# Performance work log

Measured on AMD Instinct MI355X. Metric: run time of the kernel, lower is better.

## Reference

```python
import jax, jax.numpy as jnp
import numpy as np

# irreps structure: in = 32x0e + 16x1o, hidden = 64x0e + 32x1o, out = 32x0e + 16x1o
N = 50000
S_IN, V_IN = 32, 16
S_H, V_H = 64, 32
S_OUT, V_OUT = 32, 16
INV_SQRT3 = float(1.0 / np.sqrt(3.0))  # wigner-3j for (0,1,1)/(1,0,1)/(1,1,0)
# e3nn path weights: sqrt(ir_out.dim / sum_over_paths_to_same_output(fan_in)), fan_in = mul1*mul2
PW1_S = float((1.0 / (S_IN * S_IN + V_IN * V_IN)) ** 0.5)        # sqrt(1/1280)
PW1_V = float((3.0 / (S_IN * V_IN + V_IN * S_IN)) ** 0.5)        # sqrt(3/1024)
PW2_S = float((1.0 / (S_H * S_H + V_H * V_H)) ** 0.5)            # sqrt(1/5120)
PW2_V = float((3.0 / (S_H * V_H + V_H * S_H)) ** 0.5)            # sqrt(3/4096)


def norm_act(xs, xv, bias=None, normalize=False):
    # e3nn.nn.NormActivation with sigmoid: per-irrep-channel norm, gate by sigmoid(norm [+ bias])
    ns = jnp.abs(xs)                                 # [N, S] scalar channel norms
    nv = jnp.sqrt(jnp.sum(xv * xv, axis=-1))         # [N, V] vector channel norms
    norms = jnp.concatenate([ns, nv], axis=1)        # [N, S+V]
    a = norms if bias is None else norms + bias
    f = jax.nn.sigmoid(a)
    mult = f / norms if normalize else f
    s = xs.shape[1]
    return xs * mult[:, :s], xv * mult[:, s:, None]


def fctp(xs, xv, Wsss, Wvvs, Wsvv, Wvsv, pw_s, pw_v):
    # FullyConnectedTensorProduct(x, x) restricted to 0e/1o irreps (all surviving CG paths)
    zs = pw_s * (jnp.einsum('nu,nv,uvw->nw', xs, xs, Wsss)
                 + INV_SQRT3 * jnp.einsum('nui,nvi,uvw->nw', xv, xv, Wvvs))
    zv = (pw_v * INV_SQRT3) * (jnp.einsum('nu,nvk,uvw->nwk', xs, xv, Wsvv)
                               + jnp.einsum('nuk,nv,uvw->nwk', xv, xs, Wvsv))
    return zs, zv


def setup_inputs() -> dict:
    key = jax.random.key(0)
    ks = jax.random.split(key, 11)
    return {
        'x': jax.random.normal(ks[0], (N, S_IN + 3 * V_IN), dtype=jnp.float32),
        'Wsss1': jax.random.normal(ks[1], (S_IN, S_IN, S_H), dtype=jnp.float32),
        'Wvvs1': jax.random.normal(ks[2], (V_IN, V_IN, S_H), dtype=jnp.float32),
        'Wsvv1': jax.random.normal(ks[3], (S_IN, V_IN, V_H), dtype=jnp.float32),
        'Wvsv1': jax.random.normal(ks[4], (V_IN, S_IN, V_H), dtype=jnp.float32),
        'Wsss2': jax.random.normal(ks[5], (S_H, S_H, S_OUT), dtype=jnp.float32),
        'Wvvs2': jax.random.normal(ks[6], (V_H, V_H, S_OUT), dtype=jnp.float32),
        'Wsvv2': jax.random.normal(ks[7], (S_H, V_H, V_OUT), dtype=jnp.float32),
        'Wvsv2': jax.random.normal(ks[8], (V_H, S_H, V_OUT), dtype=jnp.float32),
        'b1': 0.1 * jax.random.normal(ks[9], (S_IN + V_IN,), dtype=jnp.float32),
        'b3': 0.1 * jax.random.normal(ks[10], (S_OUT + V_OUT,), dtype=jnp.float32),
    }


def reference(x, Wsss1, Wvvs1, Wsvv1, Wvsv1, Wsss2, Wvvs2, Wsvv2, Wvsv2, b1, b3):
    xs = x[:, :S_IN]
    xv = x[:, S_IN:].reshape(-1, V_IN, 3)
    xs, xv = norm_act(xs, xv, bias=b1, normalize=False)            # non_linear_act1
    hs, hv = fctp(xs, xv, Wsss1, Wvvs1, Wsvv1, Wvsv1, PW1_S, PW1_V)  # si1
    hs, hv = norm_act(hs, hv, bias=None, normalize=True)           # normalize_and_non_linear_act2
    os_, ov = fctp(hs, hv, Wsss2, Wvvs2, Wsvv2, Wvsv2, PW2_S, PW2_V)  # si2
    os_, ov = norm_act(os_, ov, bias=b3, normalize=False)          # non_linear_act3
    return jnp.concatenate([os_, ov.reshape(-1, V_OUT * 3)], axis=1)
```

## Files before the change

kernel.cpp:

```cpp
#include <hip/hip_runtime.h>

#define NROWS 50000

typedef float f32x4 __attribute__((ext_vector_type(4)));
typedef float f32x16 __attribute__((ext_vector_type(16)));
typedef short s16x8 __attribute__((ext_vector_type(8)));
typedef _Float16 f16x8 __attribute__((ext_vector_type(8)));

#define MFMA16B(a,b,c) __builtin_amdgcn_mfma_f32_16x16x32_bf16(a, b, c, 0, 0, 0)
#define MFMA32B(a,b,c) __builtin_amdgcn_mfma_f32_32x32x16_bf16(a, b, c, 0, 0, 0)
#define MFMA32H(a,b,c) __builtin_amdgcn_mfma_f32_32x32x16_f16(a, b, c, 0, 0, 0)

#define Q1ABH 0
#define Q1ABL 81920
#define Q1CH  163840
#define Q1CL  212992
#define P2A   262144
#define P2AV  (262144 + 73728)
#define P2C   425984
#define PREPN 323584


#define LO_SCALE   2048.0f
#define LO_UNSCALE 4.8828125e-4f

__device__ __forceinline__ float sigm(float a){ return 1.0f/(1.0f+__expf(-a)); }
__device__ __forceinline__ short bfb(float f){
  __bf16 b = (__bf16)f;
  return *reinterpret_cast<short*>(&b);
}
__device__ __forceinline__ float b2f(short s){
  unsigned u = ((unsigned)(unsigned short)s) << 16;
  float f;
  __builtin_memcpy(&f, &u, 4);
  return f;
}
__device__ __forceinline__ f32x16 zero16(){
  f32x16 v;
  #pragma unroll
  for (int i = 0; i < 16; ++i) v[i] = 0.f;
  return v;
}

__global__ __launch_bounds__(256) void prep_weights(
    const float* __restrict__ Wsss1, const float* __restrict__ Wvvs1,
    const float* __restrict__ Wsvv1, const float* __restrict__ Wvsv1,
    const float* __restrict__ Wsss2, const float* __restrict__ Wvvs2,
    const float* __restrict__ Wsvv2, const float* __restrict__ Wvsv2,
    short* __restrict__ pb)
{
  const float PW1S = 0.027950849718747374f;
  const float PW2S = 0.013975424859373687f;
  const float IS3  = 0.57735026918962576f;
  int i = blockIdx.x * 256 + threadIdx.x;
  if (i >= PREPN) return;
  if (i < 131072) {
    float w;
    int hiOff, loOff;
    if (i < 81920) {
      int e = i; int j = e & 7, l = (e >> 3) & 63, st = e >> 9;
      int t = st & 1, s = st >> 1;
      int k = 16*s + 8*(l >> 5) + j, n = 32*t + (l & 31);
      if (k < 1024) { int u = k >> 5, v = k & 31; w = PW1S * Wsss1[(u*32 + v)*64 + n]; }
      else { int kk = k - 1024; int u = kk >> 4, v = kk & 15; w = PW1S * IS3 * Wvvs1[(u*16 + v)*64 + n]; }
      hiOff = Q1ABH + e; loOff = Q1ABL + e;
    } else {
      int e = i - 81920; int e2 = e & 16383;
      int j = e2 & 7, l = (e2 >> 3) & 63, s = e2 >> 9;
      int k = 16*s + 8*(l >> 5) + j, n = l & 31;
      int u = k >> 4, v = k & 15;
      w = 0.03125f * (Wsvv1[(u*16 + v)*32 + n] + Wvsv1[(v*32 + u)*32 + n]);
      hiOff = Q1CH + e; loOff = Q1CL + e;
    }
    _Float16 h = (_Float16)w;
    float r = w - (float)h;
    _Float16 lo = (_Float16)(r * LO_SCALE);
    pb[hiOff] = *reinterpret_cast<short*>(&h);
    pb[loOff] = *reinterpret_cast<short*>(&lo);
  } else {
    int e = i - 131072;
    float val; int off;
    if (e < 73728) {
      int j = e & 7, l = (e >> 3) & 63, s = e >> 9;
      int k = 16*s + 8*(l >> 5) + j, n = l & 31;
      int B = k >> 6, kb = k & 63;
      int bb = 0;
      while ((bb + 1) * (bb + 2) / 2 <= B) ++bb;
      int a = B - bb * (bb + 1) / 2;
      int u = 8*a + (kb >> 3), v = 8*bb + (kb & 7);
      float w1 = Wsss2[(u*64 + v)*32 + n];
      val = PW2S * (a == bb ? w1 : w1 + Wsss2[(v*64 + u)*32 + n]);
      off = P2A + e;
    } else if (e < 94208) {
      int e2 = e - 73728;
      int j = e2 & 7, l = (e2 >> 3) & 63, s = e2 >> 9;
      int k = 16*s + 8*(l >> 5) + j, n = l & 31;
      int B = k >> 6, kb = k & 63;
      int bb = 0;
      while ((bb + 1) * (bb + 2) / 2 <= B) ++bb;
      int a = B - bb * (bb + 1) / 2;
      int u = 8*a + (kb >> 3), v = 8*bb + (kb & 7);
      float w1 = Wvvs2[(u*32 + v)*32 + n];
      val = PW2S * IS3 * (a == bb ? w1 : w1 + Wvvs2[(v*32 + u)*32 + n]);
      off = P2AV + e2;
    } else {
      int e3 = e - 94208; int e4 = e3 & 32767;
      int j = e4 & 7, l = (e4 >> 3) & 63, s = e4 >> 9;
      int k = 32*s + 8*(l >> 4) + j, n = l & 15;
      int u = k >> 5, v = k & 31;
      val = 0.015625f * (Wsvv2[(u*32 + v)*16 + n] + Wvsv2[(v*64 + u)*16 + n]);
      off = P2C + e3;
    }
    pb[off] = bfb(val);
  }
}

__global__ __launch_bounds__(128, 4) void double_layer(
    const float* __restrict__ x,
    const float* __restrict__ b1,
    const float* __restrict__ b3,
    const short* __restrict__ pb,
    float* __restrict__ out)
{
  __shared__ __align__(16) float smem[5120];
  char* S = (char*)smem;

  const int lane = threadIdx.x & 63;
  const int wid  = __builtin_amdgcn_readfirstlane(threadIdx.x >> 6);
  const int h    = lane >> 5;
  const int r31  = lane & 31;
  const int row  = r31;
  const int grow0 = blockIdx.x * 32;
  const int xb = row * 320;
  const int hb = 10240 + row * 320;
  const int sz = ((row >> 1) & 3) << 4;
  const bool valid = (grow0 + row) < NROWS;
  const float* xrow = x + (size_t)(grow0 + row) * 80;

  if (wid == 0) {
    #pragma unroll
    for (int i = 0; i < 4; ++i) {
      float4 qv = valid ? ((const float4*)xrow)[4*h + i] : float4{0.f,0.f,0.f,0.f};
      int c0 = 16*h + 4*i;
      f32x4 o;
      o[0] = qv.x * sigm(fabsf(qv.x) + b1[c0+0]);
      o[1] = qv.y * sigm(fabsf(qv.y) + b1[c0+1]);
      o[2] = qv.z * sigm(fabsf(qv.z) + b1[c0+2]);
      o[3] = qv.w * sigm(fabsf(qv.w) + b1[c0+3]);
      *(f32x4*)(S + xb + ((64*h + 16*i) ^ sz)) = o;
    }
  } else {
    float t[24];
    #pragma unroll
    for (int i = 0; i < 6; ++i) {
      float4 qv = valid ? ((const float4*)xrow)[8 + 6*h + i] : float4{0.f,0.f,0.f,0.f};
      t[4*i] = qv.x; t[4*i+1] = qv.y; t[4*i+2] = qv.z; t[4*i+3] = qv.w;
    }
    #pragma unroll
    for (int vv = 0; vv < 8; ++vv) {
      float a0 = t[3*vv], a1 = t[3*vv+1], a2 = t[3*vv+2];
      float f = sigm(sqrtf(a0*a0 + a1*a1 + a2*a2) + b1[32 + 8*h + vv]);
      t[3*vv] = a0*f; t[3*vv+1] = a1*f; t[3*vv+2] = a2*f;
    }
    #pragma unroll
    for (int i = 0; i < 6; ++i) {
      f32x4 o; o[0] = t[4*i]; o[1] = t[4*i+1]; o[2] = t[4*i+2]; o[3] = t[4*i+3];
      *(f32x4*)(S + xb + ((128 + 96*h + 16*i) ^ sz)) = o;
    }
  }
  __syncthreads();

  if (wid == 0) {
    f32x16 aH0 = zero16(), aM0 = zero16(), aH1 = zero16(), aM1 = zero16();
    const f16x8* BH = (const f16x8*)(pb + Q1ABH);
    const f16x8* BL = (const f16x8*)(pb + Q1ABL);
    float xsv[16];
    {
      #pragma unroll
      for (int si = 0; si < 2; ++si) {
        f32x4 p0 = *(const f32x4*)(S + xb + ((64*si + 32*h) ^ sz));
        f32x4 p1 = *(const f32x4*)(S + xb + ((64*si + 32*h + 16) ^ sz));
        #pragma unroll
        for (int j = 0; j < 4; ++j) { xsv[8*si+j] = p0[j]; xsv[8*si+4+j] = p1[j]; }
      }
    }
    #pragma unroll 2
    for (int so = 0; so < 32; ++so) {
      float xu = *(const float*)(S + xb + ((4*so) ^ sz));
      #pragma unroll
      for (int si = 0; si < 2; ++si) {
        int s = 2*so + si;
        f16x8 ah, al;
        #pragma unroll
        for (int j = 0; j < 8; ++j) {
          float f = xu * xsv[8*si + j];
          _Float16 hh = (_Float16)f;
          ah[j] = hh;
          al[j] = (_Float16)((f - (float)hh) * LO_SCALE);
        }
        const f16x8* Bh = BH + (2*s)*64 + lane;
        const f16x8* Bl = BL + (2*s)*64 + lane;
        f16x8 b0 = Bh[0], b1_ = Bh[64];
        aH0 = MFMA32H(ah, b0,  aH0); aM0 = MFMA32H(al, b0,  aM0); aM0 = MFMA32H(ah, Bl[0],  aM0);
        aH1 = MFMA32H(ah, b1_, aH1); aM1 = MFMA32H(al, b1_, aM1); aM1 = MFMA32H(ah, Bl[64], aM1);
      }
    }
    {
      float pv0[8], pv1[8], pv2[8];
      f32x4 P[6];
      #pragma unroll
      for (int i = 0; i < 6; ++i) P[i] = *(const f32x4*)(S + xb + ((128 + 96*h + 16*i) ^ sz));
      #pragma unroll
      for (int j = 0; j < 8; ++j) {
        pv0[j] = P[(3*j  )>>2][(3*j  )&3];
        pv1[j] = P[(3*j+1)>>2][(3*j+1)&3];
        pv2[j] = P[(3*j+2)>>2][(3*j+2)&3];
      }
      #pragma unroll 2
      for (int s2 = 0; s2 < 16; ++s2) {
        int s = 64 + s2;
        float u0 = *(const float*)(S + xb + ((4*(32 + 3*s2    )) ^ sz));
        float u1 = *(const float*)(S + xb + ((4*(32 + 3*s2 + 1)) ^ sz));
        float u2 = *(const float*)(S + xb + ((4*(32 + 3*s2 + 2)) ^ sz));
        f16x8 ah, al;
        #pragma unroll
        for (int j = 0; j < 8; ++j) {
          float f = u0*pv0[j] + u1*pv1[j] + u2*pv2[j];
          _Float16 hh = (_Float16)f;
          ah[j] = hh;
          al[j] = (_Float16)((f - (float)hh) * LO_SCALE);
        }
        const f16x8* Bh = BH + (2*s)*64 + lane;
        const f16x8* Bl = BL + (2*s)*64 + lane;
        f16x8 b0 = Bh[0], b1_ = Bh[64];
        aH0 = MFMA32H(ah, b0,  aH0); aM0 = MFMA32H(al, b0,  aM0); aM0 = MFMA32H(ah, Bl[0],  aM0);
        aH1 = MFMA32H(ah, b1_, aH1); aM1 = MFMA32H(al, b1_, aM1); aM1 = MFMA32H(ah, Bl[64], aM1);
      }
    }
    #pragma unroll
    for (int reg = 0; reg < 16; ++reg) {
      int rowD = (reg & 3) + 8*(reg >> 2) + 4*h;
      int hbD = 10240 + rowD*320;
      int szD = ((rowD >> 1) & 3) << 4;
      float z0 = aH0[reg] + LO_UNSCALE*aM0[reg];
      float z1 = aH1[reg] + LO_UNSCALE*aM1[reg];
      *(short*)(S + hbD + ((2*r31)        ^ szD)) = bfb(copysignf(sigm(fabsf(z0)), z0));
      *(short*)(S + hbD + ((2*(32 + r31)) ^ szD)) = bfb(copysignf(sigm(fabsf(z1)), z1));
    }
  } else {
    float pv0[8], pv1[8], pv2[8];
    {
      f32x4 P[6];
      #pragma unroll
      for (int i = 0; i < 6; ++i) P[i] = *(const f32x4*)(S + xb + ((128 + 96*h + 16*i) ^ sz));
      #pragma unroll
      for (int j = 0; j < 8; ++j) {
        pv0[j] = P[(3*j  )>>2][(3*j  )&3];
        pv1[j] = P[(3*j+1)>>2][(3*j+1)&3];
        pv2[j] = P[(3*j+2)>>2][(3*j+2)&3];
      }
    }
    const f16x8* CH = (const f16x8*)(pb + Q1CH);
    const f16x8* CL = (const f16x8*)(pb + Q1CL);
    f32x16 z0v, z1v, z2v;
    {
      f32x16 cH0 = zero16(), cM0 = zero16(), cH1 = zero16(), cM1 = zero16();
      #pragma unroll 2
      for (int s = 0; s < 32; ++s) {
        float xu = *(const float*)(S + xb + ((4*s) ^ sz));
        f16x8 a0h, a0l, a1h, a1l;
        #pragma unroll
        for (int j = 0; j < 8; ++j) {
          float f0 = xu*pv0[j]; _Float16 h0 = (_Float16)f0; a0h[j] = h0; a0l[j] = (_Float16)((f0 - (float)h0)*LO_SCALE);
          float f1 = xu*pv1[j]; _Float16 h1 = (_Float16)f1; a1h[j] = h1; a1l[j] = (_Float16)((f1 - (float)h1)*LO_SCALE);
        }
        const f16x8* B0h = CH + s*64 + lane;
        const f16x8* B0l = CL + s*64 + lane;
        f16x8 t0 = B0h[0];
        cH0 = MFMA32H(a0h, t0, cH0); cM0 = MFMA32H(a0l, t0, cM0); cM0 = MFMA32H(a0h, B0l[0], cM0);
        f16x8 t1 = B0h[2048];
        cH1 = MFMA32H(a1h, t1, cH1); cM1 = MFMA32H(a1l, t1, cM1); cM1 = MFMA32H(a1h, B0l[2048], cM1);
      }
      #pragma unroll
      for (int i = 0; i < 16; ++i) { z0v[i] = cH0[i] + LO_UNSCALE*cM0[i]; z1v[i] = cH1[i] + LO_UNSCALE*cM1[i]; }
    }
    {
      f32x16 cH2 = zero16(), cM2 = zero16();
      #pragma unroll 2
      for (int s = 0; s < 32; ++s) {
        float xu = *(const float*)(S + xb + ((4*s) ^ sz));
        f16x8 a2h, a2l;
        #pragma unroll
        for (int j = 0; j < 8; ++j) {
          float f2 = xu*pv2[j]; _Float16 h2 = (_Float16)f2; a2h[j] = h2; a2l[j] = (_Float16)((f2 - (float)h2)*LO_SCALE);
        }
        const f16x8* B2h = CH + 4096 + s*64 + lane;
        const f16x8* B2l = CL + 4096 + s*64 + lane;
        f16x8 t2 = B2h[0];
        cH2 = MFMA32H(a2h, t2, cH2); cM2 = MFMA32H(a2l, t2, cM2); cM2 = MFMA32H(a2h, B2l[0], cM2);
      }
      #pragma unroll
      for (int i = 0; i < 16; ++i) z2v[i] = cH2[i] + LO_UNSCALE*cM2[i];
    }
    #pragma unroll
    for (int reg = 0; reg < 16; ++reg) {
      int rowD = (reg & 3) + 8*(reg >> 2) + 4*h;
      int hbD = 10240 + rowD*320;
      int szD = ((rowD >> 1) & 3) << 4;
      float a0 = z0v[reg], a1 = z1v[reg], a2 = z2v[reg];
      float n = sqrtf(a0*a0 + a1*a1 + a2*a2);
      float mm = sigm(n) / n;
      int ch = 64 + 3*r31;
      *(short*)(S + hbD + ((2*(ch    )) ^ szD)) = bfb(a0*mm);
      *(short*)(S + hbD + ((2*(ch + 1)) ^ szD)) = bfb(a1*mm);
      *(short*)(S + hbD + ((2*(ch + 2)) ^ szD)) = bfb(a2*mm);
    }
  }
  __syncthreads();

  if (wid == 0) {
    f32x16 acc = zero16();
    {
      const s16x8* BA = (const s16x8*)(pb + P2A);
      int step = 0;
      #pragma unroll 2
      for (int b = 0; b < 8; ++b) {
        float hsb[8];
        {
          s16x8 w = *(const s16x8*)(S + hb + ((16*b) ^ sz));
          #pragma unroll
          for (int j = 0; j < 8; ++j) hsb[j] = b2f(w[j]);
        }
        for (int a = 0; a <= b; ++a) {
          #pragma unroll
          for (int s4 = 0; s4 < 4; ++s4) {
            float hu = b2f(*(const short*)(S + hb + ((2*(8*a + 2*s4 + h)) ^ sz)));
            s16x8 av;
            #pragma unroll
            for (int j = 0; j < 8; ++j) av[j] = bfb(hu * hsb[j]);
            acc = MFMA32B(av, BA[step*64 + lane], acc);
            ++step;
          }
        }
      }
    }
    {
      const s16x8* BV = (const s16x8*)(pb + P2AV);
      int step = 0;
      #pragma unroll
      for (int b = 0; b < 4; ++b) {
        float hvb[24];
        #pragma unroll
        for (int i = 0; i < 3; ++i) {
          s16x8 w = *(const s16x8*)(S + hb + ((2*(64 + 24*b + 8*i)) ^ sz));
          #pragma unroll
          for (int j = 0; j < 8; ++j) hvb[8*i + j] = b2f(w[j]);
        }
        for (int a = 0; a <= b; ++a) {
          #pragma unroll
          for (int s4 = 0; s4 < 4; ++s4) {
            int u = 8*a + 2*s4 + h;
            float u0 = b2f(*(const short*)(S + hb + ((2*(64 + 3*u    )) ^ sz)));
            float u1 = b2f(*(const short*)(S + hb + ((2*(64 + 3*u + 1)) ^ sz)));
            float u2 = b2f(*(const short*)(S + hb + ((2*(64 + 3*u + 2)) ^ sz)));
            s16x8 av;
            #pragma unroll
            for (int j = 0; j < 8; ++j)
              av[j] = bfb(u0*hvb[3*j] + u1*hvb[3*j+1] + u2*hvb[3*j+2]);
            acc = MFMA32B(av, BV[step*64 + lane], acc);
            ++step;
          }
        }
      }
    }
    float bs = b3[r31];
    #pragma unroll
    for (int reg = 0; reg < 16; ++reg) {
      int rowD = (reg & 3) + 8*(reg >> 2) + 4*h;
      int grow = grow0 + rowD;
      if (grow < NROWS) {
        float z = acc[reg];
        out[(size_t)grow*80 + r31] = z * sigm(fabsf(z) + bs);
      }
    }
  } else {
    const int q = lane >> 4, r15 = lane & 15;
    const int rA = r15, rB = 16 + r15;
    const int hbA = 10240 + rA*320, szA = ((rA >> 1) & 3) << 4;
    const int hbB = 10240 + rB*320, szB = ((rB >> 1) & 3) << 4;
    float vvA[24], vvB[24];
    #pragma unroll
    for (int i = 0; i < 3; ++i) {
      s16x8 wa = *(const s16x8*)(S + hbA + ((128 + 48*q + 16*i) ^ szA));
      s16x8 wb = *(const s16x8*)(S + hbB + ((128 + 48*q + 16*i) ^ szB));
      #pragma unroll
      for (int j = 0; j < 8; ++j) { vvA[8*i+j] = b2f(wa[j]); vvB[8*i+j] = b2f(wb[j]); }
    }
    f32x4 ac00 = {0.f,0.f,0.f,0.f}, ac01 = {0.f,0.f,0.f,0.f};
    f32x4 ac10 = {0.f,0.f,0.f,0.f}, ac11 = {0.f,0.f,0.f,0.f};
    f32x4 ac20 = {0.f,0.f,0.f,0.f}, ac21 = {0.f,0.f,0.f,0.f};
    const s16x8* BC = (const s16x8*)(pb + P2C);
    #pragma unroll 2
    for (int s = 0; s < 64; ++s) {
      float huA = b2f(*(const short*)(S + hbA + ((2*s) ^ szA)));
      float huB = b2f(*(const short*)(S + hbB + ((2*s) ^ szB)));
      s16x8 aA0, aA1, aA2, aB0, aB1, aB2;
      #pragma unroll
      for (int j = 0; j < 8; ++j) {
        aA0[j] = bfb(huA*vvA[3*j  ]); aA1[j] = bfb(huA*vvA[3*j+1]); aA2[j] = bfb(huA*vvA[3*j+2]);
        aB0[j] = bfb(huB*vvB[3*j  ]); aB1[j] = bfb(huB*vvB[3*j+1]); aB2[j] = bfb(huB*vvB[3*j+2]);
      }
      s16x8 B0 = BC[s*64 + lane];
      s16x8 B1 = BC[4096 + s*64 + lane];
      s16x8 B2 = BC[8192 + s*64 + lane];
      ac00 = MFMA16B(aA0, B0, ac00); ac01 = MFMA16B(aB0, B0, ac01);
      ac10 = MFMA16B(aA1, B1, ac10); ac11 = MFMA16B(aB1, B1, ac11);
      ac20 = MFMA16B(aA2, B2, ac20); ac21 = MFMA16B(aB2, B2, ac21);
    }
    float bv = b3[32 + r15];
    #pragma unroll
    for (int r = 0; r < 4; ++r) {
      int gA = grow0 + 4*q + r;
      if (gA < NROWS) {
        float z0 = ac00[r], z1 = ac10[r], z2 = ac20[r];
        float gg = sigm(sqrtf(z0*z0 + z1*z1 + z2*z2) + bv);
        out[(size_t)gA*80 + 32 + 3*r15    ] = z0*gg;
        out[(size_t)gA*80 + 32 + 3*r15 + 1] = z1*gg;
        out[(size_t)gA*80 + 32 + 3*r15 + 2] = z2*gg;
      }
      int gB = grow0 + 16 + 4*q + r;
      if (gB < NROWS) {
        float z0 = ac01[r], z1 = ac11[r], z2 = ac21[r];
        float gg = sigm(sqrtf(z0*z0 + z1*z1 + z2*z2) + bv);
        out[(size_t)gB*80 + 32 + 3*r15    ] = z0*gg;
        out[(size_t)gB*80 + 32 + 3*r15 + 1] = z1*gg;
        out[(size_t)gB*80 + 32 + 3*r15 + 2] = z2*gg;
      }
    }
  }
}

extern "C" void kernel_launch(void* const* d_in, const int* in_sizes, int n_in,
                              void* d_out, int out_size, void* d_ws, size_t ws_size,
                              hipStream_t stream) {
  const float* x     = (const float*)d_in[0];
  const float* Wsss1 = (const float*)d_in[1];
  const float* Wvvs1 = (const float*)d_in[2];
  const float* Wsvv1 = (const float*)d_in[3];
  const float* Wvsv1 = (const float*)d_in[4];
  const float* Wsss2 = (const float*)d_in[5];
  const float* Wvvs2 = (const float*)d_in[6];
  const float* Wsvv2 = (const float*)d_in[7];
  const float* Wvsv2 = (const float*)d_in[8];
  const float* b1    = (const float*)d_in[9];
  const float* b3    = (const float*)d_in[10];
  float* out = (float*)d_out;
  short* pb  = (short*)d_ws;

  hipLaunchKernelGGL(prep_weights, dim3((PREPN + 255)/256), dim3(256), 0, stream,
                     Wsss1, Wvvs1, Wsvv1, Wvsv1, Wsss2, Wvvs2, Wsvv2, Wvsv2, pb);
  hipLaunchKernelGGL(double_layer, dim3((NROWS + 31)/32), dim3(128), 0, stream,
                     x, b1, b3, pb, out);
}
```

Measured before the change: 116.2 us.

## Split fused double-layer work across four waves instead of two

```diff
diff --git a/kernel.cpp b/kernel.cpp
--- a/kernel.cpp
+++ b/kernel.cpp
@@ -18,7 +18,8 @@
 #define P2A   262144
 #define P2AV  (262144 + 73728)
 #define P2C   425984
-#define PREPN 323584
+#define PREPN 393216
+
 
 
 #define LO_SCALE   2048.0f
@@ -115,7 +116,7 @@
   }
 }
 
-__global__ __launch_bounds__(128, 4) void double_layer(
+__global__ __launch_bounds__(256, 4) void double_layer(
     const float* __restrict__ x,
     const float* __restrict__ b1,
     const float* __restrict__ b3,
@@ -149,7 +150,7 @@
       o[3] = qv.w * sigm(fabsf(qv.w) + b1[c0+3]);
       *(f32x4*)(S + xb + ((64*h + 16*i) ^ sz)) = o;
     }
-  } else {
+  } else if (wid == 1) {
     float t[24];
     #pragma unroll
     for (int i = 0; i < 6; ++i) {
@@ -170,10 +171,13 @@
   }
   __syncthreads();
 
-  if (wid == 0) {
-    f32x16 aH0 = zero16(), aM0 = zero16(), aH1 = zero16(), aM1 = zero16();
+  f32x16 z0v, z1v;
+
+  if (wid == 0 || wid == 1) {
+    f32x16 aH = zero16(), aM = zero16();
     const f16x8* BH = (const f16x8*)(pb + Q1ABH);
     const f16x8* BL = (const f16x8*)(pb + Q1ABL);
+    const int toff = (wid == 0) ? 0 : 64;
     float xsv[16];
     {
       #pragma unroll
@@ -198,11 +202,10 @@
           ah[j] = hh;
           al[j] = (_Float16)((f - (float)hh) * LO_SCALE);
         }
-        const f16x8* Bh = BH + (2*s)*64 + lane;
-        const f16x8* Bl = BL + (2*s)*64 + lane;
-        f16x8 b0 = Bh[0], b1_ = Bh[64];
-        aH0 = MFMA32H(ah, b0,  aH0); aM0 = MFMA32H(al, b0,  aM0); aM0 = MFMA32H(ah, Bl[0],  aM0);
-        aH1 = MFMA32H(ah, b1_, aH1); aM1 = MFMA32H(al, b1_, aM1); aM1 = MFMA32H(ah, Bl[64], aM1);
+        const f16x8* Bh = BH + (2*s)*64 + lane + toff;
+        const f16x8* Bl = BL + (2*s)*64 + lane + toff;
+        f16x8 b0 = Bh[0];
+        aH = MFMA32H(ah, b0, aH); aM = MFMA32H(al, b0, aM); aM = MFMA32H(ah, Bl[0], aM);
       }
     }
     {
@@ -230,25 +233,23 @@
           ah[j] = hh;
           al[j] = (_Float16)((f - (float)hh) * LO_SCALE);
         }
-        const f16x8* Bh = BH + (2*s)*64 + lane;
-        const f16x8* Bl = BL + (2*s)*64 + lane;
-        f16x8 b0 = Bh[0], b1_ = Bh[64];
-        aH0 = MFMA32H(ah, b0,  aH0); aM0 = MFMA32H(al, b0,  aM0); aM0 = MFMA32H(ah, Bl[0],  aM0);
-        aH1 = MFMA32H(ah, b1_, aH1); aM1 = MFMA32H(al, b1_, aM1); aM1 = MFMA32H(ah, Bl[64], aM1);
-      }
-    }
+        const f16x8* Bh = BH + (2*s)*64 + lane + toff;
+        const f16x8* Bl = BL + (2*s)*64 + lane + toff;
+        f16x8 b0 = Bh[0];
+        aH = MFMA32H(ah, b0, aH); aM = MFMA32H(al, b0, aM); aM = MFMA32H(ah, Bl[0], aM);
+      }
+    }
+    const int choff = (wid == 0) ? 0 : 32;
     #pragma unroll
     for (int reg = 0; reg < 16; ++reg) {
       int rowD = (reg & 3) + 8*(reg >> 2) + 4*h;
       int hbD = 10240 + rowD*320;
       int szD = ((rowD >> 1) & 3) << 4;
-      float z0 = aH0[reg] + LO_UNSCALE*aM0[reg];
-      float z1 = aH1[reg] + LO_UNSCALE*aM1[reg];
-      *(short*)(S + hbD + ((2*r31)        ^ szD)) = bfb(copysignf(sigm(fabsf(z0)), z0));
-      *(short*)(S + hbD + ((2*(32 + r31)) ^ szD)) = bfb(copysignf(sigm(fabsf(z1)), z1));
-    }
-  } else {
-    float pv0[8], pv1[8], pv2[8];
+      float z = aH[reg] + LO_UNSCALE*aM[reg];
+      *(short*)(S + hbD + ((2*(choff + r31)) ^ szD)) = bfb(copysignf(sigm(fabsf(z)), z));
+    }
+  } else if (wid == 2) {
+    float pv0[8], pv1[8];
     {
       f32x4 P[6];
       #pragma unroll
@@ -257,57 +258,78 @@
       for (int j = 0; j < 8; ++j) {
         pv0[j] = P[(3*j  )>>2][(3*j  )&3];
         pv1[j] = P[(3*j+1)>>2][(3*j+1)&3];
-        pv2[j] = P[(3*j+2)>>2][(3*j+2)&3];
       }
     }
     const f16x8* CH = (const f16x8*)(pb + Q1CH);
     const f16x8* CL = (const f16x8*)(pb + Q1CL);
-    f32x16 z0v, z1v, z2v;
+    f32x16 cH0 = zero16(), cM0 = zero16(), cH1 = zero16(), cM1 = zero16();
+    #pragma unroll 2
+    for (int s = 0; s < 32; ++s) {
+      float xu = *(const float*)(S + xb + ((4*s) ^ sz));
+      f16x8 a0h, a0l, a1h, a1l;
+      #pragma unroll
+      for (int j = 0; j < 8; ++j) {
+        float f0 = xu*pv0[j]; _Float16 h0 = (_Float16)f0; a0h[j] = h0; a0l[j] = (_Float16)((f0 - (float)h0)*LO_SCALE);
+        float f1 = xu*pv1[j]; _Float16 h1 = (_Float16)f1; a1h[j] = h1; a1l[j] = (_Float16)((f1 - (float)h1)*LO_SCALE);
+      }
+      const f16x8* B0h = CH + s*64 + lane;
+      const f16x8* B0l = CL + s*64 + lane;
+      f16x8 t0 = B0h[0];
+      cH0 = MFMA32H(a0h, t0, cH0); cM0 = MFMA32H(a0l, t0, cM0); cM0 = MFMA32H(a0h, B0l[0], cM0);
+      f16x8 t1 = B0h[2048];
+      cH1 = MFMA32H(a1h, t1, cH1); cM1 = MFMA32H(a1l, t1, cM1); cM1 = MFMA32H(a1h, B0l[2048], cM1);
+    }
+    #pragma unroll
+    for (int i = 0; i < 16; ++i) { z0v[i] = cH0[i] + LO_UNSCALE*cM0[i]; z1v[i] = cH1[i] + LO_UNSCALE*cM1[i]; }
+  } else {
+    float pv2[8];
     {
-      f32x16 cH0 = zero16(), cM0 = zero16(), cH1 = zero16(), cM1 = zero16();
-      #pragma unroll 2
-      for (int s = 0; s < 32; ++s) {
-        float xu = *(const float*)(S + xb + ((4*s) ^ sz));
-        f16x8 a0h, a0l, a1h, a1l;
-        #pragma unroll
-        for (int j = 0; j < 8; ++j) {
-          float f0 = xu*pv0[j]; _Float16 h0 = (_Float16)f0; a0h[j] = h0; a0l[j] = (_Float16)((f0 - (float)h0)*LO_SCALE);
-          float f1 = xu*pv1[j]; _Float16 h1 = (_Float16)f1; a1h[j] = h1; a1l[j] = (_Float16)((f1 - (float)h1)*LO_SCALE);
-        }
-        const f16x8* B0h = CH + s*64 + lane;
-        const f16x8* B0l = CL + s*64 + lane;
-        f16x8 t0 = B0h[0];
-        cH0 = MFMA32H(a0h, t0, cH0); cM0 = MFMA32H(a0l, t0, cM0); cM0 = MFMA32H(a0h, B0l[0], cM0);
-        f16x8 t1 = B0h[2048];
-        cH1 = MFMA32H(a1h, t1, cH1); cM1 = MFMA32H(a1l, t1, cM1); cM1 = MFMA32H(a1h, B0l[2048], cM1);
-      }
-      #pragma unroll
-      for (int i = 0; i < 16; ++i) { z0v[i] = cH0[i] + LO_UNSCALE*cM0[i]; z1v[i] = cH1[i] + LO_UNSCALE*cM1[i]; }
-    }
-    {
-      f32x16 cH2 = zero16(), cM2 = zero16();
-      #pragma unroll 2
-      for (int s = 0; s < 32; ++s) {
-        float xu = *(const float*)(S + xb + ((4*s) ^ sz));
-        f16x8 a2h, a2l;
-        #pragma unroll
-        for (int j = 0; j < 8; ++j) {
-          float f2 = xu*pv2[j]; _Float16 h2 = (_Float16)f2; a2h[j] = h2; a2l[j] = (_Float16)((f2 - (float)h2)*LO_SCALE);
-        }
-        const f16x8* B2h = CH + 4096 + s*64 + lane;
-        const f16x8* B2l = CL + 4096 + s*64 + lane;
-        f16x8 t2 = B2h[0];
-        cH2 = MFMA32H(a2h, t2, cH2); cM2 = MFMA32H(a2l, t2, cM2); cM2 = MFMA32H(a2h, B2l[0], cM2);
-      }
-      #pragma unroll
-      for (int i = 0; i < 16; ++i) z2v[i] = cH2[i] + LO_UNSCALE*cM2[i];
+      f32x4 P[6];
+      #pragma unroll
+      for (int i = 0; i < 6; ++i) P[i] = *(const f32x4*)(S + xb + ((128 + 96*h + 16*i) ^ sz));
+      #pragma unroll
+      for (int j = 0; j < 8; ++j)
+        pv2[j] = P[(3*j+2)>>2][(3*j+2)&3];
+    }
+    const f16x8* CH = (const f16x8*)(pb + Q1CH);
+    const f16x8* CL = (const f16x8*)(pb + Q1CL);
+    f32x16 cH2 = zero16(), cM2 = zero16();
+    #pragma unroll 2
+    for (int s = 0; s < 32; ++s) {
+      float xu = *(const float*)(S + xb + ((4*s) ^ sz));
+      f16x8 a2h, a2l;
+      #pragma unroll
+      for (int j = 0; j < 8; ++j) {
+        float f2 = xu*pv2[j]; _Float16 h2 = (_Float16)f2; a2h[j] = h2; a2l[j] = (_Float16)((f2 - (float)h2)*LO_SCALE);
+      }
+      const f16x8* B2h = CH + 4096 + s*64 + lane;
+      const f16x8* B2l = CL + 4096 + s*64 + lane;
+      f16x8 t2 = B2h[0];
+      cH2 = MFMA32H(a2h, t2, cH2); cM2 = MFMA32H(a2l, t2, cM2); cM2 = MFMA32H(a2h, B2l[0], cM2);
+    }
+    #pragma unroll
+    for (int reg = 0; reg < 16; ++reg) {
+      int rowD = (reg & 3) + 8*(reg >> 2) + 4*h;
+      float z2 = cH2[reg] + LO_UNSCALE*cM2[reg];
+      *(float*)(S + 10240 + rowD*320 + 128 + 4*r31) = z2;
+    }
+  }
+  __syncthreads();
+
+  f32x16 acc = zero16();
+  if (wid == 2) {
+    float z2a[16];
+    #pragma unroll
+    for (int reg = 0; reg < 16; ++reg) {
+      int rowD = (reg & 3) + 8*(reg >> 2) + 4*h;
+      z2a[reg] = *(const float*)(S + 10240 + rowD*320 + 128 + 4*r31);
     }
     #pragma unroll
     for (int reg = 0; reg < 16; ++reg) {
       int rowD = (reg & 3) + 8*(reg >> 2) + 4*h;
       int hbD = 10240 + rowD*320;
       int szD = ((rowD >> 1) & 3) << 4;
-      float a0 = z0v[reg], a1 = z1v[reg], a2 = z2v[reg];
+      float a0 = z0v[reg], a1 = z1v[reg], a2 = z2a[reg];
       float n = sqrtf(a0*a0 + a1*a1 + a2*a2);
       float mm = sigm(n) / n;
       int ch = 64 + 3*r31;
@@ -315,35 +337,41 @@
       *(short*)(S + hbD + ((2*(ch + 1)) ^ szD)) = bfb(a1*mm);
       *(short*)(S + hbD + ((2*(ch + 2)) ^ szD)) = bfb(a2*mm);
     }
+  } else {
+    const s16x8* BA = (const s16x8*)(pb + P2A);
+    int bLo, bHi, step;
+    if (wid == 0)      { bLo = 0; bHi = 5; step = 0;   }
+    else if (wid == 1) { bLo = 5; bHi = 7; step = 60;  }
+    else               { bLo = 7; bHi = 8; step = 112; }
+    for (int b = bLo; b < bHi; ++b) {
+      float hsb[8];
+      {
+        s16x8 w = *(const s16x8*)(S + hb + ((16*b) ^ sz));
+        #pragma unroll
+        for (int j = 0; j < 8; ++j) hsb[j] = b2f(w[j]);
+      }
+      for (int a = 0; a <= b; ++a) {
+        #pragma unroll
+        for (int s4 = 0; s4 < 4; ++s4) {
+          float hu = b2f(*(const short*)(S + hb + ((2*(8*a + 2*s4 + h)) ^ sz)));
+          s16x8 av;
+          #pragma unroll
+          for (int j = 0; j < 8; ++j) av[j] = bfb(hu * hsb[j]);
+          acc = MFMA32B(av, BA[step*64 + lane], acc);
+          ++step;
+        }
+      }
+    }
+    if (wid == 1 || wid == 3) {
+      int slot = (wid == 1) ? 0 : 4096;
+      #pragma unroll
+      for (int reg = 0; reg < 16; ++reg)
+        *(float*)(S + slot + (reg*64 + lane)*4) = acc[reg];
+    }
   }
   __syncthreads();
 
   if (wid == 0) {
-    f32x16 acc = zero16();
-    {
-      const s16x8* BA = (const s16x8*)(pb + P2A);
-      int step = 0;
-      #pragma unroll 2
-      for (int b = 0; b < 8; ++b) {
-        float hsb[8];
-        {
-          s16x8 w = *(const s16x8*)(S + hb + ((16*b) ^ sz));
-          #pragma unroll
-          for (int j = 0; j < 8; ++j) hsb[j] = b2f(w[j]);
-        }
-        for (int a = 0; a <= b; ++a) {
-          #pragma unroll
-          for (int s4 = 0; s4 < 4; ++s4) {
-            float hu = b2f(*(const short*)(S + hb + ((2*(8*a + 2*s4 + h)) ^ sz)));
-            s16x8 av;
-            #pragma unroll
-            for (int j = 0; j < 8; ++j) av[j] = bfb(hu * hsb[j]);
-            acc = MFMA32B(av, BA[step*64 + lane], acc);
-            ++step;
-          }
-        }
-      }
-    }
     {
       const s16x8* BV = (const s16x8*)(pb + P2AV);
       int step = 0;
@@ -373,6 +401,10 @@
         }
       }
     }
+    #pragma unroll
+    for (int reg = 0; reg < 16; ++reg)
+      acc[reg] += *(const float*)(S + (reg*64 + lane)*4)
+                + *(const float*)(S + 4096 + (reg*64 + lane)*4);
     float bs = b3[r31];
     #pragma unroll
     for (int reg = 0; reg < 16; ++reg) {
@@ -383,7 +415,7 @@
         out[(size_t)grow*80 + r31] = z * sigm(fabsf(z) + bs);
       }
     }
-  } else {
+  } else if (wid == 2) {
     const int q = lane >> 4, r15 = lane & 15;
     const int rA = r15, rB = 16 + r15;
     const int hbA = 10240 + rA*320, szA = ((rA >> 1) & 3) << 4;
@@ -459,6 +491,6 @@
 
   hipLaunchKernelGGL(prep_weights, dim3((PREPN + 255)/256), dim3(256), 0, stream,
                      Wsss1, Wvvs1, Wsvv1, Wvsv1, Wsss2, Wvvs2, Wsvv2, Wvsv2, pb);
-  hipLaunchKernelGGL(double_layer, dim3((NROWS + 31)/32), dim3(128), 0, stream,
+  hipLaunchKernelGGL(double_layer, dim3((NROWS + 31)/32), dim3(256), 0, stream,
                      x, b1, b3, pb, out);
 }
```

After: 141.2 us. 21.6% more time.

## Split fused double-layer kernel into two launches via global hidden buffer

Applied to the files above, without the earlier changes.

```diff
diff --git a/kernel.cpp b/kernel.cpp
--- a/kernel.cpp
+++ b/kernel.cpp
@@ -1,6 +1,7 @@
 #include <hip/hip_runtime.h>
 
 #define NROWS 50000
+#define NTILES ((NROWS + 31) / 32)
 
 typedef float f32x4 __attribute__((ext_vector_type(4)));
 typedef float f32x16 __attribute__((ext_vector_type(16)));
@@ -18,7 +19,8 @@
 #define P2A   262144
 #define P2AV  (262144 + 73728)
 #define P2C   425984
-#define PREPN 323584
+#define PREPN 393216
+#define HWSOFF 524288
 
 
 #define LO_SCALE   2048.0f
@@ -115,24 +117,13 @@
   }
 }
 
-__global__ __launch_bounds__(128, 4) void double_layer(
-    const float* __restrict__ x,
-    const float* __restrict__ b1,
-    const float* __restrict__ b3,
-    const short* __restrict__ pb,
-    float* __restrict__ out)
+__device__ __forceinline__ void l1_body(
+    const float* __restrict__ x, const float* __restrict__ b1,
+    const short* __restrict__ pb, char* S,
+    int lane, int wid, int h, int r31, int grow0)
 {
-  __shared__ __align__(16) float smem[5120];
-  char* S = (char*)smem;
-
-  const int lane = threadIdx.x & 63;
-  const int wid  = __builtin_amdgcn_readfirstlane(threadIdx.x >> 6);
-  const int h    = lane >> 5;
-  const int r31  = lane & 31;
-  const int row  = r31;
-  const int grow0 = blockIdx.x * 32;
+  const int row = r31;
   const int xb = row * 320;
-  const int hb = 10240 + row * 320;
   const int sz = ((row >> 1) & 3) << 4;
   const bool valid = (grow0 + row) < NROWS;
   const float* xrow = x + (size_t)(grow0 + row) * 80;
@@ -317,6 +308,15 @@
     }
   }
   __syncthreads();
+}
+
+__device__ __forceinline__ void l2_body(
+    const float* __restrict__ b3, const short* __restrict__ pb, char* S,
+    float* __restrict__ out, int lane, int wid, int h, int r31, int grow0)
+{
+  const int row = r31;
+  const int hb = 10240 + row * 320;
+  const int sz = ((row >> 1) & 3) << 4;
 
   if (wid == 0) {
     f32x16 acc = zero16();
@@ -438,6 +438,76 @@
       }
     }
   }
+}
+
+__global__ __launch_bounds__(128, 4) void double_layer_l1(
+    const float* __restrict__ x,
+    const float* __restrict__ b1,
+    const short* __restrict__ pb,
+    short* __restrict__ hws)
+{
+  __shared__ __align__(16) float smem[5120];
+  char* S = (char*)smem;
+  const int lane = threadIdx.x & 63;
+  const int wid  = __builtin_amdgcn_readfirstlane(threadIdx.x >> 6);
+  const int h    = lane >> 5;
+  const int r31  = lane & 31;
+  const int grow0 = blockIdx.x * 32;
+
+  l1_body(x, b1, pb, S, lane, wid, h, r31, grow0);
+
+  const s16x8* src = (const s16x8*)(S + 10240);
+  s16x8* dst = (s16x8*)(hws + (size_t)blockIdx.x * 5120);
+  int tid = threadIdx.x;
+  #pragma unroll
+  for (int i = 0; i < 5; ++i)
+    dst[tid + 128*i] = src[tid + 128*i];
+}
+
+__global__ __launch_bounds__(128, 4) void double_layer_l2(
+    const float* __restrict__ b3,
+    const short* __restrict__ pb,
+    const short* __restrict__ hws,
+    float* __restrict__ out)
+{
+  __shared__ __align__(16) float smem[5120];
+  char* S = (char*)smem;
+  const int lane = threadIdx.x & 63;
+  const int wid  = __builtin_amdgcn_readfirstlane(threadIdx.x >> 6);
+  const int h    = lane >> 5;
+  const int r31  = lane & 31;
+  const int grow0 = blockIdx.x * 32;
+
+  {
+    const s16x8* src = (const s16x8*)(hws + (size_t)blockIdx.x * 5120);
+    s16x8* dst = (s16x8*)(S + 10240);
+    int tid = threadIdx.x;
+    #pragma unroll
+    for (int i = 0; i < 5; ++i)
+      dst[tid + 128*i] = src[tid + 128*i];
+  }
+  __syncthreads();
+
+  l2_body(b3, pb, S, out, lane, wid, h, r31, grow0);
+}
+
+__global__ __launch_bounds__(128, 4) void double_layer(
+    const float* __restrict__ x,
+    const float* __restrict__ b1,
+    const float* __restrict__ b3,
+    const short* __restrict__ pb,
+    float* __restrict__ out)
+{
+  __shared__ __align__(16) float smem[5120];
+  char* S = (char*)smem;
+  const int lane = threadIdx.x & 63;
+  const int wid  = __builtin_amdgcn_readfirstlane(threadIdx.x >> 6);
+  const int h    = lane >> 5;
+  const int r31  = lane & 31;
+  const int grow0 = blockIdx.x * 32;
+
+  l1_body(x, b1, pb, S, lane, wid, h, r31, grow0);
+  l2_body(b3, pb, S, out, lane, wid, h, r31, grow0);
 }
 
 extern "C" void kernel_launch(void* const* d_in, const int* in_sizes, int n_in,
@@ -459,6 +529,16 @@
 
   hipLaunchKernelGGL(prep_weights, dim3((PREPN + 255)/256), dim3(256), 0, stream,
                      Wsss1, Wvvs1, Wsvv1, Wvsv1, Wsss2, Wvvs2, Wsvv2, Wvsv2, pb);
-  hipLaunchKernelGGL(double_layer, dim3((NROWS + 31)/32), dim3(128), 0, stream,
-                     x, b1, b3, pb, out);
-}
+
+  const size_t needBytes = (size_t)HWSOFF * 2 + (size_t)NTILES * 10240;
+  if (ws_size >= needBytes) {
+    short* hws = pb + HWSOFF;
+    hipLaunchKernelGGL(double_layer_l1, dim3(NTILES), dim3(128), 0, stream,
+                       x, b1, pb, hws);
+    hipLaunchKernelGGL(double_layer_l2, dim3(NTILES), dim3(128), 0, stream,
+                       b3, pb, hws, out);
+  } else {
+    hipLaunchKernelGGL(double_layer, dim3(NTILES), dim3(128), 0, stream,
+                       x, b1, b3, pb, out);
+  }
+}
```

After: 119.0 us. +2.4%, slower.
